# Kernel optimization log

Measured on AMD Instinct MI355X. Metric: run time of the kernel, lower is better.

Reference implementation:

```python
import jax, jax.numpy as jnp
import numpy as np
from jax import lax

C = 64   # channels
R = 2    # SKM expansion ratio
M = 4    # number of dilated convs
EPS = 1e-6


def conv3_dilated(x, w, b, d):
    # 3x3 conv, dilation d, padding d (same spatial size)
    y = lax.conv_general_dilated(x, w, (1, 1), [(d, d), (d, d)],
                                 rhs_dilation=(d, d),
                                 dimension_numbers=('NCHW', 'OIHW', 'NCHW'))
    return y + b[None, :, None, None]


def ln2d(x, g, b):
    # LayerNorm over channel dim at each spatial position (NAFNet LayerNorm2d)
    mu = x.mean(1, keepdims=True)
    var = x.var(1, keepdims=True)
    return (x - mu) / jnp.sqrt(var + EPS) * g[None, :, None, None] + b[None, :, None, None]


def skm(x, dw, db, c1w, c1b, pw):
    # dw: [M,C,C,3,3], db: [M,C], c1w: [R*C,C], c1b: [R*C], pw: [R*C, M*C]
    D = jnp.stack([conv3_dilated(x, dw[i], db[i], 2 * (i + 1)) for i in range(M)])  # [M,B,C,H,W]
    Z = D.sum(0).mean((-2, -1))                      # [B,C] global avg pool of summed branches
    S = jax.nn.relu(Z @ c1w.T + c1b)                 # [B,R*C]
    Sw = jax.nn.softmax((S @ pw).reshape(-1, M, C), axis=-1)  # [B,M,C], softmax over C
    return jnp.einsum('mbchw,bmc->bchw', D, Sw)      # weighted sum of branches


def setup_inputs() -> dict:
    key = jax.random.key(0)
    ks = jax.random.split(key, 24)
    B, H, W = 4, 96, 256
    sc = 0.05
    inp = {
        'x_l': jax.random.normal(ks[0], (B, C, H, W), jnp.float32),
        'x_r': jax.random.normal(ks[1], (B, C, H, W), jnp.float32),
        'lnl_g': jnp.ones((C,), jnp.float32),
        'lnl_b': jnp.zeros((C,), jnp.float32),
        'lnr_g': jnp.ones((C,), jnp.float32),
        'lnr_b': jnp.zeros((C,), jnp.float32),
        'l_dw': jax.random.normal(ks[2], (M, C, C, 3, 3), jnp.float32) * sc,
        'l_db': jax.random.normal(ks[3], (M, C), jnp.float32) * sc,
        'l_c1w': jax.random.normal(ks[4], (R * C, C), jnp.float32) * sc,
        'l_c1b': jax.random.normal(ks[5], (R * C,), jnp.float32) * sc,
        'l_pw': jax.random.normal(ks[6], (R * C, M * C), jnp.float32) * sc,
        'r_dw': jax.random.normal(ks[7], (M, C, C, 3, 3), jnp.float32) * sc,
        'r_db': jax.random.normal(ks[8], (M, C), jnp.float32) * sc,
        'r_c1w': jax.random.normal(ks[9], (R * C, C), jnp.float32) * sc,
        'r_c1b': jax.random.normal(ks[10], (R * C,), jnp.float32) * sc,
        'r_pw': jax.random.normal(ks[11], (R * C, M * C), jnp.float32) * sc,
        'l2w': jax.random.normal(ks[12], (C, C), jnp.float32) * sc,
        'l2b': jax.random.normal(ks[13], (C,), jnp.float32) * sc,
        'r2w': jax.random.normal(ks[14], (C, C), jnp.float32) * sc,
        'r2b': jax.random.normal(ks[15], (C,), jnp.float32) * sc,
        'beta': jax.random.normal(ks[16], (1, C, 1, 1), jnp.float32) * sc,
        'gamma': jax.random.normal(ks[17], (1, C, 1, 1), jnp.float32) * sc,
    }
    return inp


def reference(x_l, x_r, lnl_g, lnl_b, lnr_g, lnr_b,
              l_dw, l_db, l_c1w, l_c1b, l_pw,
              r_dw, r_db, r_c1w, r_c1b, r_pw,
              l2w, l2b, r2w, r2b, beta, gamma):
    scale = C ** (-0.5)
    Ql = skm(ln2d(x_l, lnl_g, lnl_b), l_dw, l_db, l_c1w, l_c1b, l_pw).transpose(0, 2, 3, 1)  # [B,H,W,C]
    Qr = skm(ln2d(x_r, lnr_g, lnr_b), r_dw, r_db, r_c1w, r_c1b, r_pw).transpose(0, 2, 3, 1)  # [B,H,W,C]
    Vl = (jnp.einsum('bchw,dc->bdhw', x_l, l2w) + l2b[None, :, None, None]).transpose(0, 2, 3, 1)
    Vr = (jnp.einsum('bchw,dc->bdhw', x_r, r2w) + r2b[None, :, None, None]).transpose(0, 2, 3, 1)
    attn = jnp.einsum('bhwc,bhvc->bhwv', Ql, Qr) * scale  # shared score matrix [B,H,W,W]
    F_r2l = jnp.einsum('bhwv,bhvc->bhwc', jax.nn.softmax(attn, axis=-1), Vr).transpose(0, 3, 1, 2)
    F_l2r = jnp.einsum('bhwv,bhwc->bhvc', jax.nn.softmax(attn, axis=-2), Vl).transpose(0, 3, 1, 2)
    return x_l + F_r2l * beta, x_r + F_l2r * gamma
```

## Files before the change

kernel.cpp:

```cpp
#include <hip/hip_runtime.h>
#include <hip/hip_bf16.h>
#include <cstdint>

constexpr int NB = 4;
constexpr int NC = 64;
constexpr int NH = 96;
constexpr int NW = 256;
constexpr int HWp = NH * NW;
constexpr float EPS = 1e-6f;

typedef __attribute__((ext_vector_type(8))) short short8;
typedef __attribute__((ext_vector_type(4))) short short4t;
typedef __attribute__((ext_vector_type(4))) float f32x4;

static __device__ __forceinline__ short f2bf(float f) {
    __hip_bfloat16 h = __float2bfloat16(f);
    return *reinterpret_cast<short*>(&h);
}

__global__ __launch_bounds__(256) void k_ln(const float* __restrict__ x_l,
                                            const float* __restrict__ x_r,
                                            const float* __restrict__ gl,
                                            const float* __restrict__ bl,
                                            const float* __restrict__ gr,
                                            const float* __restrict__ br,
                                            short* __restrict__ XBl,
                                            short* __restrict__ XBr,
                                            float* __restrict__ R) {
    const int h = blockIdx.x, sideb = blockIdx.y;
    const int side = sideb >> 2, b = sideb & 3;
    const float* x = side ? x_r : x_l;
    const float* g = side ? gr : gl;
    const float* bta = side ? br : bl;
    short* XB = side ? XBr : XBl;
    const int t = threadIdx.x;
    __shared__ float xm[32 * 256];

    const float* xp = x + ((size_t)b * NC * NH + h) * NW + t;
    float v[64];
    float s = 0.f, sq = 0.f;
#pragma unroll
    for (int c = 0; c < 64; ++c) {
        float tv = xp[(size_t)c * HWp];
        v[c] = tv; s += tv; sq += tv * tv;
    }
    float mu = s * (1.f / 64.f);
    float var = sq * (1.f / 64.f) - mu * mu;
    float rs = rsqrtf(var + EPS);
#pragma unroll
    for (int c = 0; c < 64; ++c) v[c] = (v[c] - mu) * rs * g[c] + bta[c];

#pragma unroll
    for (int chunk = 0; chunk < 4; ++chunk) {
        short8 s0, s1;
#pragma unroll
        for (int j = 0; j < 8; ++j) {
            s0[j] = f2bf(v[chunk * 16 + j]);
            s1[j] = f2bf(v[chunk * 16 + 8 + j]);
        }
        short* xb = XB + (((size_t)(b * 4 + chunk) * NH + h) * NW + t) * 16;
        *(short8*)xb = s0;
        *(short8*)(xb + 8) = s1;
    }

#pragma unroll
    for (int p = 0; p < 2; ++p) {
        const int cbase = p * 32;
        __syncthreads();
#pragma unroll
        for (int c = 0; c < 32; ++c)
            xm[c * 256 + (((t >> 2) ^ (c & 7)) << 2) + (t & 3)] = v[cbase + c];
        __syncthreads();
        const int cc = t & 31, q = t >> 5;
        float rsum = 0.f;
        float4 fs0 = {0,0,0,0}, fs1 = {0,0,0,0}, ls0 = {0,0,0,0}, ls1 = {0,0,0,0};
#pragma unroll
        for (int i = 0; i < 8; ++i) {
            int j4 = q * 8 + i;
            float4 f = *(const float4*)&xm[cc * 256 + ((j4 ^ (cc & 7)) << 2)];
            rsum += (f.x + f.y) + (f.z + f.w);
            if (i == 0) fs0 = f;
            if (i == 1) fs1 = f;
            if (i == 6) ls0 = f;
            if (i == 7) ls1 = f;
        }
        __syncthreads();
        xm[cc * 8 + q] = rsum;
        if (q == 7) {
            *(float4*)&xm[256 + cc * 8] = ls0;
            *(float4*)&xm[256 + cc * 8 + 4] = ls1;
        }
        __syncthreads();
        if (t < 32) {
            const int c = t;
            float full = 0.f;
#pragma unroll
            for (int q2 = 0; q2 < 8; ++q2) full += xm[c * 8 + q2];
            float h0 = xm[256 + c * 8 + 0], h1 = xm[256 + c * 8 + 1];
            float h2 = xm[256 + c * 8 + 2], h3 = xm[256 + c * 8 + 3];
            float h4 = xm[256 + c * 8 + 4], h5 = xm[256 + c * 8 + 5];
            float h6 = xm[256 + c * 8 + 6], h7 = xm[256 + c * 8 + 7];
            float e2 = fs0.x + fs0.y;
            float e4 = e2 + fs0.z + fs0.w;
            float e6 = e4 + fs1.x + fs1.y;
            float e8 = e6 + fs1.z + fs1.w;
            float r2 = h6 + h7;
            float r4 = (h4 + h5) + r2;
            float r6 = r4 + (h2 + h3);
            float r8 = r6 + (h0 + h1);
            float* Rp = R + ((size_t)(sideb * 64 + cbase + c) * NH + h) * 9;
            Rp[0] = full; Rp[1] = e2; Rp[2] = e4; Rp[3] = e6; Rp[4] = e8;
            Rp[5] = r2;  Rp[6] = r4; Rp[7] = r6; Rp[8] = r8;
        }
    }
}

__global__ __launch_bounds__(128) void k_comb(const float* __restrict__ R,
                                              float* __restrict__ T) {
    int x = blockIdx.x;
    int side = x >> 8, rem = x & 255, b = rem >> 6, ci = rem & 63;
    __shared__ float rp[NH][9];
    int t = threadIdx.x;
    const float* src = R + (size_t)x * NH * 9;
    for (int i = t; i < NH * 9; i += 128) ((float*)rp)[i] = src[i];
    __syncthreads();
    if (t < 36) {
        int m = t / 9, kh = (t % 9) / 3, kw = t % 3;
        int d = 2 * (m + 1);
        int r0 = (kh == 2) ? d : 0;
        int r1 = (kh == 0) ? NH - d : NH;
        float s = 0.f;
        for (int r = r0; r < r1; ++r) {
            float rowv = rp[r][0];
            if (kw == 0) rowv -= rp[r][5 + m];
            else if (kw == 2) rowv -= rp[r][1 + m];
            s += rowv;
        }
        T[side * 9216 + (b * 4 + m) * 576 + ci * 9 + kh * 3 + kw] = s;
    }
}

__global__ __launch_bounds__(256) void k_z(const float* __restrict__ T,
                                           const float* __restrict__ l_dw,
                                           const float* __restrict__ r_dw,
                                           const float* __restrict__ l_db,
                                           const float* __restrict__ r_db,
                                           float* __restrict__ Z) {
    int x = blockIdx.x;
    int side = x >> 8, bc = x & 255;
    int b = bc >> 6, c = bc & 63;
    const float* dw = side ? r_dw : l_dw;
    const float* db = side ? r_db : l_db;
    int t = threadIdx.x, lane = t & 63, m = t >> 6;
    const float* wp = dw + (size_t)(m * 64 + c) * 576;
    const float* tp = T + side * 9216 + (size_t)(b * 4 + m) * 576;
    float s = 0.f;
    for (int j = lane; j < 576; j += 64) s += wp[j] * tp[j];
#pragma unroll
    for (int o = 32; o; o >>= 1) s += __shfl_xor(s, o, 64);
    __shared__ float red[4];
    if (lane == 0) red[m] = s;
    __syncthreads();
    if (t == 0) {
        float z = (red[0] + red[1]) + (red[2] + red[3]);
        float bias = db[c] + db[64 + c] + db[128 + c] + db[192 + c];
        Z[x] = z * (1.f / (float)HWp) + bias;
    }
}

__global__ __launch_bounds__(256) void k_sel2(const float* __restrict__ Z,
                                              const float* __restrict__ l_db,
                                              const float* __restrict__ r_db,
                                              const float* __restrict__ l_c1w,
                                              const float* __restrict__ r_c1w,
                                              const float* __restrict__ l_c1b,
                                              const float* __restrict__ r_c1b,
                                              const float* __restrict__ l_pw,
                                              const float* __restrict__ r_pw,
                                              float* __restrict__ Sw,
                                              float* __restrict__ Qb) {
    int x = blockIdx.x;
    int side = x >> 2;
    const float* db  = side ? r_db  : l_db;
    const float* c1w = side ? r_c1w : l_c1w;
    const float* c1b = side ? r_c1b : l_c1b;
    const float* pw  = side ? r_pw  : l_pw;
    int t = threadIdx.x, lane = t & 63, wv = t >> 6;
    __shared__ float zs[64], ss[128], sw[256];
    __shared__ float cw[128 * 64];
    if (t < 64) zs[t] = Z[x * 64 + t];
    for (int i = t; i < 8192; i += 256) cw[i] = c1w[i];
    __syncthreads();
    if (t < 128) {
        float s = c1b[t];
        const float* wrow = cw + t * 64;
        for (int c = 0; c < 64; ++c) s += zs[c] * wrow[c];
        ss[t] = fmaxf(s, 0.f);
    }
    __syncthreads();
    float p = 0.f;
    for (int j = 0; j < 128; ++j) p += ss[j] * pw[j * 256 + t];
    float mx = p;
#pragma unroll
    for (int o = 32; o; o >>= 1) mx = fmaxf(mx, __shfl_xor(mx, o, 64));
    float e = __expf(p - mx);
    float sum = e;
#pragma unroll
    for (int o = 32; o; o >>= 1) sum += __shfl_xor(sum, o, 64);
    float swv = e / sum;
    Sw[(x * 4 + wv) * 64 + lane] = swv;
    sw[wv * 64 + lane] = swv;
    __syncthreads();
    if (t < 64) {
        float qb = sw[t] * db[t] + sw[64 + t] * db[64 + t]
                 + sw[128 + t] * db[128 + t] + sw[192 + t] * db[192 + t];
        Qb[x * 64 + t] = qb;
    }
}

__global__ __launch_bounds__(256) void k_fold(const float* __restrict__ l_dw,
                                              const float* __restrict__ r_dw,
                                              const float* __restrict__ Sw,
                                              short* __restrict__ WB) {
    int bx = blockIdx.x;
    int side = (bx >= 2304) ? 1 : 0;
    int idx = (bx - side * 2304) * 256 + threadIdx.x;
    const float* dw = side ? r_dw : l_dw;
    short* wbs = WB + (size_t)side * 589824;
    int kk = idx & 31;
    int co = (idx >> 5) & 63;
    int rest = idx >> 11;
    int tpair = rest % 18;
    int bc = rest / 18;
    int chunk = bc & 3, b = bc >> 2;
    int tpl = kk >> 4, cil = kk & 15;
    int tap = 2 * tpair + tpl;
    int m = tap / 9, k9 = tap % 9;
    int ci = chunk * 16 + cil;
    float val = Sw[((side * 4 + b) * 4 + m) * 64 + co]
              * dw[(size_t)((m * 64 + co) * 64 + ci) * 9 + k9];
    wbs[idx] = f2bf(val);
}

__global__ __launch_bounds__(256) void k_convm(const short* __restrict__ XBl,
                                               const short* __restrict__ XBr,
                                               const short* __restrict__ WBa,
                                               const float* __restrict__ QBa,
                                               short* __restrict__ QLs,
                                               short* __restrict__ QRs) {
    const int wt = blockIdx.x, h = blockIdx.y;
    const int side = blockIdx.z >> 2, b = blockIdx.z & 3;
    const short* XB = side ? XBr : XBl;
    const short* WB = WBa + (size_t)side * 589824;
    const float* Qb = QBa + side * 256;
    short* Qs = side ? QRs : QLs;
    const int t = threadIdx.x;
    const int lane = t & 63, wave = t >> 6;
    const int g = lane >> 4, ln15 = lane & 15;
    __shared__ short tile[2 * 9 * 144 * 8];

    f32x4 acc[2][4];
    {
        float qb[4];
#pragma unroll
        for (int nt = 0; nt < 4; ++nt) qb[nt] = Qb[b * 64 + nt * 16 + ln15];
#pragma unroll
        for (int mt = 0; mt < 2; ++mt)
#pragma unroll
            for (int nt = 0; nt < 4; ++nt)
                acc[mt][nt] = (f32x4){qb[nt], qb[nt], qb[nt], qb[nt]};
    }
    const int w0 = wt * 128;
    const int laneelem = (wave * 32 + ln15) * 8;
    const int halfoff = (g & 1) * (9 * 144 * 8);
    const int tsel = g >> 1;

    short8 pv[6][2];
    auto LOADC = [&](int chunk) {
        const short* src = XB + (size_t)(b * 4 + chunk) * NH * NW * 16;
#pragma unroll
        for (int i = 0; i < 6; ++i) {
            const int slot = t + i * 256;
            const bool live = (i < 5) || (t < 16);
            short8 z = {0, 0, 0, 0, 0, 0, 0, 0};
            pv[i][0] = z; pv[i][1] = z;
            if (live) {
                int r = slot / 144, col = slot % 144;
                int gh = h + 2 * r - 8;
                int gw = w0 - 8 + col;
                if (gh >= 0 && gh < NH && gw >= 0 && gw < NW) {
                    const short* p = src + ((size_t)gh * NW + gw) * 16;
                    pv[i][0] = *(const short8*)p;
                    pv[i][1] = *(const short8*)(p + 8);
                }
            }
        }
    };

    LOADC(0);
    for (int chunk = 0; chunk < 4; ++chunk) {
        __builtin_amdgcn_s_barrier();
        __builtin_amdgcn_sched_barrier(0);
#pragma unroll
        for (int i = 0; i < 6; ++i) {
            const int slot = t + i * 256;
            const bool live = (i < 5) || (t < 16);
            if (live) {
                *(short8*)(tile + slot * 8) = pv[i][0];
                *(short8*)(tile + (9 * 144 + slot) * 8) = pv[i][1];
            }
        }
        if (chunk < 3) LOADC(chunk + 1);
        asm volatile("s_waitcnt lgkmcnt(0)" ::: "memory");
        __builtin_amdgcn_s_barrier();
        __builtin_amdgcn_sched_barrier(0);

        const short* wbase = WB + (size_t)((b * 4 + chunk) * 18) * 2048 + ln15 * 32 + g * 8;
        for (int tp = 0; tp < 18; ++tp) {
            int ta = 2 * tp, tb = ta + 1;
            int ma = ta / 9, k9a = ta % 9;
            int mb = tb / 9, k9b = tb % 9;
            int offA = ((4 + (ma + 1) * (k9a / 3 - 1)) * 144 + 8 + 2 * (ma + 1) * (k9a % 3 - 1)) * 8;
            int offB = ((4 + (mb + 1) * (k9b / 3 - 1)) * 144 + 8 + 2 * (mb + 1) * (k9b % 3 - 1)) * 8;
            int aoff = (tsel ? offB : offA) + laneelem + halfoff;
            const short* ap = tile + aoff;
            short8 a0 = *(const short8*)(ap);
            short8 a1 = *(const short8*)(ap + 128);
            const short* bp = wbase + (size_t)tp * 2048;
            short8 b0 = *(const short8*)(bp);
            short8 b1 = *(const short8*)(bp + 512);
            short8 b2 = *(const short8*)(bp + 1024);
            short8 b3 = *(const short8*)(bp + 1536);
            acc[0][0] = __builtin_amdgcn_mfma_f32_16x16x32_bf16(a0, b0, acc[0][0], 0, 0, 0);
            acc[0][1] = __builtin_amdgcn_mfma_f32_16x16x32_bf16(a0, b1, acc[0][1], 0, 0, 0);
            acc[0][2] = __builtin_amdgcn_mfma_f32_16x16x32_bf16(a0, b2, acc[0][2], 0, 0, 0);
            acc[0][3] = __builtin_amdgcn_mfma_f32_16x16x32_bf16(a0, b3, acc[0][3], 0, 0, 0);
            acc[1][0] = __builtin_amdgcn_mfma_f32_16x16x32_bf16(a1, b0, acc[1][0], 0, 0, 0);
            acc[1][1] = __builtin_amdgcn_mfma_f32_16x16x32_bf16(a1, b1, acc[1][1], 0, 0, 0);
            acc[1][2] = __builtin_amdgcn_mfma_f32_16x16x32_bf16(a1, b2, acc[1][2], 0, 0, 0);
            acc[1][3] = __builtin_amdgcn_mfma_f32_16x16x32_bf16(a1, b3, acc[1][3], 0, 0, 0);
        }
    }
#pragma unroll
    for (int mt = 0; mt < 2; ++mt) {
        int px = w0 + wave * 32 + mt * 16 + g * 4;
#pragma unroll
        for (int j = 0; j < 4; ++j) {
            short* qp = Qs + ((size_t)(b * NH + h) * NW + px + j) * 64 + ln15;
            qp[0]  = f2bf(acc[mt][0][j]);
            qp[16] = f2bf(acc[mt][1][j]);
            qp[32] = f2bf(acc[mt][2][j]);
            qp[48] = f2bf(acc[mt][3][j]);
        }
    }
}

__global__ __launch_bounds__(256) void k_v(const float* __restrict__ x_l,
                                           const float* __restrict__ x_r,
                                           const float* __restrict__ w2l,
                                           const float* __restrict__ b2l,
                                           const float* __restrict__ w2r,
                                           const float* __restrict__ b2r,
                                           short* __restrict__ VL,
                                           short* __restrict__ VR) {
    int wt = blockIdx.x, h = blockIdx.y;
    int side = blockIdx.z >> 2, b = blockIdx.z & 3;
    const float* x  = side ? x_r : x_l;
    const float* w2 = side ? w2r : w2l;
    const float* b2 = side ? b2r : b2l;
    short* VT = side ? VR : VL;
    int t = threadIdx.x, lane = t & 63, q = t >> 6;
    __shared__ float xs[64 * 68];
    __shared__ float w2t[64 * 68];
    int w0 = wt * 64;
    const float* src = x + (size_t)(b * 64) * HWp + h * NW + w0;
    for (int idx = t; idx < 4096; idx += 256) {
        int ci = idx >> 6, col = idx & 63;
        xs[ci * 68 + col] = src[(size_t)ci * HWp + col];
    }
    for (int idx = t; idx < 4096; idx += 256) {
        int co = idx >> 6, ci = idx & 63;
        w2t[ci * 68 + co] = w2[co * 64 + ci];
    }
    __syncthreads();

    const int pl0 = (lane & 15) * 4;
    const int c0 = q * 16 + (lane >> 4) * 4;
    f32x4 a4[4];
#pragma unroll
    for (int cc = 0; cc < 4; ++cc) {
        float bb = b2[c0 + cc];
        a4[cc] = (f32x4){bb, bb, bb, bb};
    }
    for (int ci = 0; ci < 64; ++ci) {
        f32x4 xv = *(const f32x4*)(xs + ci * 68 + pl0);
        f32x4 wv = *(const f32x4*)(w2t + ci * 68 + c0);
        a4[0] += xv * wv[0];
        a4[1] += xv * wv[1];
        a4[2] += xv * wv[2];
        a4[3] += xv * wv[3];
    }
    __syncthreads();
#pragma unroll
    for (int cc = 0; cc < 4; ++cc)
        *(f32x4*)(xs + (c0 + cc) * 68 + pl0) = a4[cc];
    __syncthreads();
    {
        int s = t & 63, g2 = t >> 6;
        int u = (s >> 2) + 16 * (s & 3);
#pragma unroll
        for (int cc = 0; cc < 16; ++cc) {
            int ch = g2 * 16 + cc;
            VT[((size_t)(b * 64 + ch) * NH + h) * NW + w0 + s] = f2bf(xs[ch * 68 + u]);
        }
    }
}

__global__ __launch_bounds__(128, 2) void k_attn(const short* __restrict__ QL,
                                                 const short* __restrict__ QR,
                                                 const short* __restrict__ VL,
                                                 const short* __restrict__ VR,
                                                 const float* __restrict__ x_l,
                                                 const float* __restrict__ x_r,
                                                 const float* __restrict__ beta,
                                                 const float* __restrict__ gamma,
                                                 float* __restrict__ out_all) {
    const int bx = blockIdx.x, h = blockIdx.y;
    const int side = blockIdx.z >> 2, b = blockIdx.z & 3;
    constexpr size_t PLANE = (size_t)NB * NC * NH * NW;
    const short* Qa  = side ? QR : QL;
    const short* Qbp = side ? QL : QR;
    const short* VT  = side ? VL : VR;
    const float* xres = side ? x_r : x_l;
    const float* scl  = side ? gamma : beta;
    float* out = out_all + (side ? PLANE : 0);

    const int t = threadIdx.x, lane = t & 63, wave = t >> 6;
    const int q = lane >> 4, c15 = lane & 15;
    __shared__ __align__(16) short PB[2][32 * 72];
    short* pb = PB[wave];

    const int wbase = bx * 64 + wave * 32;
    const short* qabase = Qa + ((size_t)(b * NH + h) * NW + wbase) * 64;
    const short* qbbase = Qbp + ((size_t)(b * NH + h) * NW) * 64;

    short8 afrag[2][2];
#pragma unroll
    for (int mt = 0; mt < 2; ++mt)
#pragma unroll
        for (int kk = 0; kk < 2; ++kk)
            afrag[mt][kk] = *(const short8*)(qabase + (mt * 16 + c15) * 64 + kk * 32 + q * 8);

    f32x4 osum[2][4];
#pragma unroll
    for (int mt = 0; mt < 2; ++mt)
#pragma unroll
        for (int nt = 0; nt < 4; ++nt) osum[mt][nt] = (f32x4){0.f, 0.f, 0.f, 0.f};
    float mrow[8], lrow[8];
#pragma unroll
    for (int i = 0; i < 8; ++i) { mrow[i] = -1e30f; lrow[i] = 0.f; }

    for (int vt = 0; vt < 4; ++vt) {
        f32x4 s[2][4];
#pragma unroll
        for (int mt = 0; mt < 2; ++mt)
#pragma unroll
            for (int nt = 0; nt < 4; ++nt) s[mt][nt] = (f32x4){0.f, 0.f, 0.f, 0.f};
#pragma unroll
        for (int kk = 0; kk < 2; ++kk) {
            short8 bq[4];
#pragma unroll
            for (int nt = 0; nt < 4; ++nt)
                bq[nt] = *(const short8*)(qbbase + (size_t)(vt * 64 + nt * 16 + c15) * 64 + kk * 32 + q * 8);
#pragma unroll
            for (int mt = 0; mt < 2; ++mt)
#pragma unroll
                for (int nt = 0; nt < 4; ++nt)
                    s[mt][nt] = __builtin_amdgcn_mfma_f32_16x16x32_bf16(afrag[mt][kk], bq[nt], s[mt][nt], 0, 0, 0);
        }
#pragma unroll
        for (int mt = 0; mt < 2; ++mt)
#pragma unroll
            for (int nt = 0; nt < 4; ++nt)
#pragma unroll
                for (int r = 0; r < 4; ++r) s[mt][nt][r] *= 0.125f;
        float al[8];
#pragma unroll
        for (int mt = 0; mt < 2; ++mt)
#pragma unroll
            for (int r = 0; r < 4; ++r) {
                float m0 = fmaxf(fmaxf(s[mt][0][r], s[mt][1][r]), fmaxf(s[mt][2][r], s[mt][3][r]));
#pragma unroll
                for (int msk = 1; msk < 16; msk <<= 1) m0 = fmaxf(m0, __shfl_xor(m0, msk, 64));
                int i = mt * 4 + r;
                float mn = fmaxf(mrow[i], m0);
                al[i] = __expf(mrow[i] - mn);
                mrow[i] = mn;
            }
#pragma unroll
        for (int mt = 0; mt < 2; ++mt)
#pragma unroll
            for (int r = 0; r < 4; ++r) {
                int i = mt * 4 + r;
                float m = mrow[i];
                float p0 = __expf(s[mt][0][r] - m);
                float p1 = __expf(s[mt][1][r] - m);
                float p2 = __expf(s[mt][2][r] - m);
                float p3 = __expf(s[mt][3][r] - m);
                short4t pk = {f2bf(p0), f2bf(p1), f2bf(p2), f2bf(p3)};
                *(short4t*)(pb + (mt * 16 + q * 4 + r) * 72 + c15 * 4) = pk;
                float lsv = (p0 + p1) + (p2 + p3);
#pragma unroll
                for (int msk = 1; msk < 16; msk <<= 1) lsv += __shfl_xor(lsv, msk, 64);
                lrow[i] = lrow[i] * al[i] + lsv;
            }
#pragma unroll
        for (int mt = 0; mt < 2; ++mt)
#pragma unroll
            for (int nt = 0; nt < 4; ++nt)
#pragma unroll
                for (int r = 0; r < 4; ++r) osum[mt][nt][r] *= al[mt * 4 + r];
#pragma unroll
        for (int kk = 0; kk < 2; ++kk) {
            short8 ap[2], bv[4];
#pragma unroll
            for (int mt = 0; mt < 2; ++mt)
                ap[mt] = *(const short8*)(pb + (mt * 16 + c15) * 72 + kk * 32 + q * 8);
#pragma unroll
            for (int nt = 0; nt < 4; ++nt)
                bv[nt] = *(const short8*)(VT + ((size_t)(b * 64 + nt * 16 + c15) * NH + h) * NW + vt * 64 + kk * 32 + q * 8);
#pragma unroll
            for (int mt = 0; mt < 2; ++mt)
#pragma unroll
                for (int nt = 0; nt < 4; ++nt)
                    osum[mt][nt] = __builtin_amdgcn_mfma_f32_16x16x32_bf16(ap[mt], bv[nt], osum[mt][nt], 0, 0, 0);
        }
    }
    float linv[8];
#pragma unroll
    for (int i = 0; i < 8; ++i) linv[i] = 1.f / lrow[i];
#pragma unroll
    for (int nt = 0; nt < 4; ++nt) {
        int c = nt * 16 + c15;
        float bv = scl[c];
        size_t pbase = ((size_t)(b * 64 + c) * NH + h) * NW + wbase;
#pragma unroll
        for (int mt = 0; mt < 2; ++mt)
#pragma unroll
            for (int r = 0; r < 4; ++r) {
                size_t o = pbase + mt * 16 + q * 4 + r;
                out[o] = xres[o] + osum[mt][nt][r] * linv[mt * 4 + r] * bv;
            }
    }
}

extern "C" void kernel_launch(void* const* d_in, const int* in_sizes, int n_in,
                              void* d_out, int out_size, void* d_ws, size_t ws_size,
                              hipStream_t stream) {
    const float* x_l   = (const float*)d_in[0];
    const float* x_r   = (const float*)d_in[1];
    const float* lnl_g = (const float*)d_in[2];
    const float* lnl_b = (const float*)d_in[3];
    const float* lnr_g = (const float*)d_in[4];
    const float* lnr_b = (const float*)d_in[5];
    const float* l_dw  = (const float*)d_in[6];
    const float* l_db  = (const float*)d_in[7];
    const float* l_c1w = (const float*)d_in[8];
    const float* l_c1b = (const float*)d_in[9];
    const float* l_pw  = (const float*)d_in[10];
    const float* r_dw  = (const float*)d_in[11];
    const float* r_db  = (const float*)d_in[12];
    const float* r_c1w = (const float*)d_in[13];
    const float* r_c1b = (const float*)d_in[14];
    const float* r_pw  = (const float*)d_in[15];
    const float* l2w   = (const float*)d_in[16];
    const float* l2b   = (const float*)d_in[17];
    const float* r2w   = (const float*)d_in[18];
    const float* r2b   = (const float*)d_in[19];
    const float* beta  = (const float*)d_in[20];
    const float* gamma = (const float*)d_in[21];
    float* out = (float*)d_out;

    constexpr size_t PLANE = (size_t)NB * NC * NH * NW;
    float* ws = (float*)d_ws;
    short* XBl = (short*)ws;         ws += PLANE / 2;
    short* XBr = (short*)ws;         ws += PLANE / 2;
    short* QLs = (short*)ws;         ws += PLANE / 2;
    short* QRs = (short*)ws;         ws += PLANE / 2;
    short* VLs = (short*)ws;         ws += PLANE / 2;
    short* VRs = (short*)ws;         ws += PLANE / 2;
    short* WB  = (short*)ws;         ws += 589824;
    float* Rb  = ws;                 ws += 442368;
    float* Tb  = ws;                 ws += 18432;
    float* SW  = ws;                 ws += 2048;
    float* QB  = ws;                 ws += 512;
    float* Zb  = ws;                 ws += 512;

    dim3 blk(256);
    k_ln    <<<dim3(NH, 2 * NB), blk, 0, stream>>>(x_l, x_r, lnl_g, lnl_b, lnr_g, lnr_b,
                                                   XBl, XBr, Rb);
    k_comb  <<<dim3(512), dim3(128), 0, stream>>>(Rb, Tb);
    k_z     <<<dim3(512), blk, 0, stream>>>(Tb, l_dw, r_dw, l_db, r_db, Zb);
    k_sel2  <<<dim3(8), blk, 0, stream>>>(Zb, l_db, r_db, l_c1w, r_c1w,
                                          l_c1b, r_c1b, l_pw, r_pw, SW, QB);
    k_fold  <<<dim3(4608), blk, 0, stream>>>(l_dw, r_dw, SW, WB);
    k_convm <<<dim3(2, NH, 2 * NB), blk, 0, stream>>>(XBl, XBr, WB, QB, QLs, QRs);
    k_v     <<<dim3(4, NH, 2 * NB), blk, 0, stream>>>(x_l, x_r, l2w, l2b, r2w, r2b, VLs, VRs);
    k_attn  <<<dim3(4, NH, 2 * NB), dim3(128), 0, stream>>>(QLs, QRs, VLs, VRs,
                                                            x_l, x_r, beta, gamma, out);
}
```

Measured before the change: 372.8 us.

## Fuse comb, z and selection kernels into one mid kernel; unroll conv tap loop

Merges the three small kernels k_comb, k_z and k_sel2 into a single 8-block kernel k_mid. It computes the tap sums in shared memory, reduces them against the conv weights to get Z, then runs the selection MLP and softmax, which removes two launches and the global round trips for T and Z. In exchange, the work moves from 512-block grids to only 8 blocks, and each thread serially reads 576 weights per dot product, so this stage loses parallelism. It also fully unrolls the 18-step tap loop in the MFMA conv kernel and moves the B loads ahead of the A loads to help scheduling.

```diff
diff --git a/kernel.cpp b/kernel.cpp
--- a/kernel.cpp
+++ b/kernel.cpp
@@ -115,85 +115,84 @@
     }
 }
 
-__global__ __launch_bounds__(128) void k_comb(const float* __restrict__ R,
-                                              float* __restrict__ T) {
-    int x = blockIdx.x;
-    int side = x >> 8, rem = x & 255, b = rem >> 6, ci = rem & 63;
-    __shared__ float rp[NH][9];
-    int t = threadIdx.x;
-    const float* src = R + (size_t)x * NH * 9;
-    for (int i = t; i < NH * 9; i += 128) ((float*)rp)[i] = src[i];
-    __syncthreads();
-    if (t < 36) {
-        int m = t / 9, kh = (t % 9) / 3, kw = t % 3;
-        int d = 2 * (m + 1);
-        int r0 = (kh == 2) ? d : 0;
-        int r1 = (kh == 0) ? NH - d : NH;
-        float s = 0.f;
-        for (int r = r0; r < r1; ++r) {
-            float rowv = rp[r][0];
-            if (kw == 0) rowv -= rp[r][5 + m];
-            else if (kw == 2) rowv -= rp[r][1 + m];
-            s += rowv;
-        }
-        T[side * 9216 + (b * 4 + m) * 576 + ci * 9 + kh * 3 + kw] = s;
-    }
-}
-
-__global__ __launch_bounds__(256) void k_z(const float* __restrict__ T,
-                                           const float* __restrict__ l_dw,
-                                           const float* __restrict__ r_dw,
-                                           const float* __restrict__ l_db,
-                                           const float* __restrict__ r_db,
-                                           float* __restrict__ Z) {
-    int x = blockIdx.x;
-    int side = x >> 8, bc = x & 255;
-    int b = bc >> 6, c = bc & 63;
-    const float* dw = side ? r_dw : l_dw;
-    const float* db = side ? r_db : l_db;
-    int t = threadIdx.x, lane = t & 63, m = t >> 6;
-    const float* wp = dw + (size_t)(m * 64 + c) * 576;
-    const float* tp = T + side * 9216 + (size_t)(b * 4 + m) * 576;
-    float s = 0.f;
-    for (int j = lane; j < 576; j += 64) s += wp[j] * tp[j];
-#pragma unroll
-    for (int o = 32; o; o >>= 1) s += __shfl_xor(s, o, 64);
-    __shared__ float red[4];
-    if (lane == 0) red[m] = s;
-    __syncthreads();
-    if (t == 0) {
-        float z = (red[0] + red[1]) + (red[2] + red[3]);
-        float bias = db[c] + db[64 + c] + db[128 + c] + db[192 + c];
-        Z[x] = z * (1.f / (float)HWp) + bias;
-    }
-}
-
-__global__ __launch_bounds__(256) void k_sel2(const float* __restrict__ Z,
-                                              const float* __restrict__ l_db,
-                                              const float* __restrict__ r_db,
-                                              const float* __restrict__ l_c1w,
-                                              const float* __restrict__ r_c1w,
-                                              const float* __restrict__ l_c1b,
-                                              const float* __restrict__ r_c1b,
-                                              const float* __restrict__ l_pw,
-                                              const float* __restrict__ r_pw,
-                                              float* __restrict__ Sw,
-                                              float* __restrict__ Qb) {
-    int x = blockIdx.x;
-    int side = x >> 2;
+__global__ __launch_bounds__(256) void k_mid(const float* __restrict__ R,
+                                             const float* __restrict__ l_dw,
+                                             const float* __restrict__ r_dw,
+                                             const float* __restrict__ l_db,
+                                             const float* __restrict__ r_db,
+                                             const float* __restrict__ l_c1w,
+                                             const float* __restrict__ r_c1w,
+                                             const float* __restrict__ l_c1b,
+                                             const float* __restrict__ r_c1b,
+                                             const float* __restrict__ l_pw,
+                                             const float* __restrict__ r_pw,
+                                             float* __restrict__ Sw,
+                                             float* __restrict__ Qb) {
+    const int sideb = blockIdx.x;
+    const int side = sideb >> 2;
+    const float* dw  = side ? r_dw  : l_dw;
     const float* db  = side ? r_db  : l_db;
     const float* c1w = side ? r_c1w : l_c1w;
     const float* c1b = side ? r_c1b : l_c1b;
     const float* pw  = side ? r_pw  : l_pw;
-    int t = threadIdx.x, lane = t & 63, wv = t >> 6;
-    __shared__ float zs[64], ss[128], sw[256];
-    __shared__ float cw[128 * 64];
-    if (t < 64) zs[t] = Z[x * 64 + t];
-    for (int i = t; i < 8192; i += 256) cw[i] = c1w[i];
+    const int t = threadIdx.x, lane = t & 63, wv = t >> 6;
+
+    __shared__ float smem[11200];
+    float* region1 = smem;
+    float* Tl   = smem + 8192;
+    float* zred = Tl + 2304;
+    float* zs   = zred + 256;
+    float* ss   = zs + 64;
+    float* swl  = ss + 128;
+
+    const float* Rbase = R + (size_t)(sideb * 64) * NH * 9;
+    for (int cg = 0; cg < 8; ++cg) {
+        __syncthreads();
+        for (int i = t; i < 8 * 864; i += 256) {
+            int ci8 = i / 864, rem = i - ci8 * 864;
+            region1[ci8 * 869 + rem] = Rbase[(size_t)(cg * 8 + ci8) * 864 + rem];
+        }
+        __syncthreads();
+        for (int tau = t; tau < 288; tau += 256) {
+            int ci8 = tau / 36, tap = tau % 36;
+            int m = tap / 9, kh = (tap % 9) / 3, kw = tap % 3;
+            int d = 2 * (m + 1);
+            int r0 = (kh == 2) ? d : 0;
+            int r1 = (kh == 0) ? NH - d : NH;
+            const float* rp = region1 + ci8 * 869;
+            float s = 0.f;
+            for (int r = r0; r < r1; ++r) {
+                float rowv = rp[r * 9];
+                if (kw == 0) rowv -= rp[r * 9 + 5 + m];
+                else if (kw == 2) rowv -= rp[r * 9 + 1 + m];
+                s += rowv;
+            }
+            Tl[m * 576 + (cg * 8 + ci8) * 9 + kh * 3 + kw] = s;
+        }
+    }
+    __syncthreads();
+
+    {
+        const int m = t >> 6, c = t & 63;
+        const float* wp = dw + (size_t)(m * 64 + c) * 576;
+        const float* tp = Tl + m * 576;
+        float s = 0.f;
+        for (int j = 0; j < 576; ++j) s += wp[j] * tp[j];
+        zred[m * 64 + c] = s;
+    }
+    __syncthreads();
+    if (t < 64) {
+        float z = (zred[t] + zred[64 + t]) + (zred[128 + t] + zred[192 + t]);
+        float bias = db[t] + db[64 + t] + db[128 + t] + db[192 + t];
+        zs[t] = z * (1.f / (float)HWp) + bias;
+    }
+    __syncthreads();
+
+    for (int i = t; i < 8192; i += 256) region1[i] = c1w[i];
     __syncthreads();
     if (t < 128) {
         float s = c1b[t];
-        const float* wrow = cw + t * 64;
+        const float* wrow = region1 + t * 64;
         for (int c = 0; c < 64; ++c) s += zs[c] * wrow[c];
         ss[t] = fmaxf(s, 0.f);
     }
@@ -208,13 +207,13 @@
 #pragma unroll
     for (int o = 32; o; o >>= 1) sum += __shfl_xor(sum, o, 64);
     float swv = e / sum;
-    Sw[(x * 4 + wv) * 64 + lane] = swv;
-    sw[wv * 64 + lane] = swv;
+    Sw[(sideb * 4 + wv) * 64 + lane] = swv;
+    swl[wv * 64 + lane] = swv;
     __syncthreads();
     if (t < 64) {
-        float qb = sw[t] * db[t] + sw[64 + t] * db[64 + t]
-                 + sw[128 + t] * db[128 + t] + sw[192 + t] * db[192 + t];
-        Qb[x * 64 + t] = qb;
+        float qb = swl[t] * db[t] + swl[64 + t] * db[64 + t]
+                 + swl[128 + t] * db[128 + t] + swl[192 + t] * db[192 + t];
+        Qb[sideb * 64 + t] = qb;
     }
 }
 
@@ -316,21 +315,22 @@
         __builtin_amdgcn_sched_barrier(0);
 
         const short* wbase = WB + (size_t)((b * 4 + chunk) * 18) * 2048 + ln15 * 32 + g * 8;
+#pragma unroll
         for (int tp = 0; tp < 18; ++tp) {
-            int ta = 2 * tp, tb = ta + 1;
-            int ma = ta / 9, k9a = ta % 9;
-            int mb = tb / 9, k9b = tb % 9;
-            int offA = ((4 + (ma + 1) * (k9a / 3 - 1)) * 144 + 8 + 2 * (ma + 1) * (k9a % 3 - 1)) * 8;
-            int offB = ((4 + (mb + 1) * (k9b / 3 - 1)) * 144 + 8 + 2 * (mb + 1) * (k9b % 3 - 1)) * 8;
-            int aoff = (tsel ? offB : offA) + laneelem + halfoff;
-            const short* ap = tile + aoff;
-            short8 a0 = *(const short8*)(ap);
-            short8 a1 = *(const short8*)(ap + 128);
+            const int ta = 2 * tp, tb = ta + 1;
+            const int ma = ta / 9, k9a = ta % 9;
+            const int mb = tb / 9, k9b = tb % 9;
+            const int offA = ((4 + (ma + 1) * (k9a / 3 - 1)) * 144 + 8 + 2 * (ma + 1) * (k9a % 3 - 1)) * 8;
+            const int offB = ((4 + (mb + 1) * (k9b / 3 - 1)) * 144 + 8 + 2 * (mb + 1) * (k9b % 3 - 1)) * 8;
+            const int aoff = (tsel ? offB : offA) + laneelem + halfoff;
             const short* bp = wbase + (size_t)tp * 2048;
             short8 b0 = *(const short8*)(bp);
             short8 b1 = *(const short8*)(bp + 512);
             short8 b2 = *(const short8*)(bp + 1024);
             short8 b3 = *(const short8*)(bp + 1536);
+            const short* ap = tile + aoff;
+            short8 a0 = *(const short8*)(ap);
+            short8 a1 = *(const short8*)(ap + 128);
             acc[0][0] = __builtin_amdgcn_mfma_f32_16x16x32_bf16(a0, b0, acc[0][0], 0, 0, 0);
             acc[0][1] = __builtin_amdgcn_mfma_f32_16x16x32_bf16(a0, b1, acc[0][1], 0, 0, 0);
             acc[0][2] = __builtin_amdgcn_mfma_f32_16x16x32_bf16(a0, b2, acc[0][2], 0, 0, 0);
@@ -591,18 +591,15 @@
     short* VRs = (short*)ws;         ws += PLANE / 2;
     short* WB  = (short*)ws;         ws += 589824;
     float* Rb  = ws;                 ws += 442368;
-    float* Tb  = ws;                 ws += 18432;
     float* SW  = ws;                 ws += 2048;
     float* QB  = ws;                 ws += 512;
-    float* Zb  = ws;                 ws += 512;
 
     dim3 blk(256);
     k_ln    <<<dim3(NH, 2 * NB), blk, 0, stream>>>(x_l, x_r, lnl_g, lnl_b, lnr_g, lnr_b,
                                                    XBl, XBr, Rb);
-    k_comb  <<<dim3(512), dim3(128), 0, stream>>>(Rb, Tb);
-    k_z     <<<dim3(512), blk, 0, stream>>>(Tb, l_dw, r_dw, l_db, r_db, Zb);
-    k_sel2  <<<dim3(8), blk, 0, stream>>>(Zb, l_db, r_db, l_c1w, r_c1w,
-                                          l_c1b, r_c1b, l_pw, r_pw, SW, QB);
+    k_mid   <<<dim3(8), blk, 0, stream>>>(Rb, l_dw, r_dw, l_db, r_db,
+                                          l_c1w, r_c1w, l_c1b, r_c1b, l_pw, r_pw,
+                                          SW, QB);
     k_fold  <<<dim3(4608), blk, 0, stream>>>(l_dw, r_dw, SW, WB);
     k_convm <<<dim3(2, NH, 2 * NB), blk, 0, stream>>>(XBl, XBr, WB, QB, QLs, QRs);
     k_v     <<<dim3(4, NH, 2 * NB), blk, 0, stream>>>(x_l, x_r, l2w, l2b, r2w, r2b, VLs, VRs);
```

Result: slower. 585.0 us (+56.9%).
